# Optimization experiments

Hardware: AMD Instinct MI355X
Metric: run time of the kernel (lower is better)

The kernel has to match this reference:

```python
import jax, jax.numpy as jnp
import numpy as np

TAU = 2.0      # LIF membrane time constant
K = 2          # MaxPool1d kernel/stride
ALPHA = 4.0    # spikingjelly surrogate.Sigmoid default alpha
EPS = 1e-5     # BatchNorm1d eps
VTH = 1.0      # LIF v_threshold default

@jax.custom_vjp
def spike(x):
    # Heaviside forward, sigmoid surrogate gradient (spikingjelly surrogate.Sigmoid)
    return (x >= 0.0).astype(x.dtype)

def _spike_fwd(x):
    return spike(x), x

def _spike_bwd(x, g):
    s = jax.nn.sigmoid(ALPHA * x)
    return (g * ALPHA * s * (1.0 - s),)

spike.defvjp(_spike_fwd, _spike_bwd)


def setup_inputs() -> dict:
    key = jax.random.key(0)
    k1, k2 = jax.random.split(key)
    T, B, N, D, O = 4, 32, 1024, 512, 512
    x = jax.random.normal(k1, (T, B, N, D), jnp.float32)
    W = jax.random.normal(k2, (O, D), jnp.float32) * 0.02
    gamma = jnp.ones((O,), jnp.float32)
    beta = jnp.zeros((O,), jnp.float32)
    running_mean = jnp.zeros((O,), jnp.float32)
    running_var = jnp.ones((O,), jnp.float32)
    return {"x": x, "W": W, "gamma": gamma, "beta": beta,
            "running_mean": running_mean, "running_var": running_var}


def reference(x, W, gamma, beta, running_mean, running_var):
    T, B, N, D = x.shape
    O = W.shape[0]
    # Linear (no bias): [T,B,N,D] x [O,D] -> [T,B,N,O]
    h = jnp.einsum('tbnd,od->tbno', x, W)
    # BatchNorm1d in inference form (running stats), fused affine
    inv = gamma * jax.lax.rsqrt(running_var + EPS)
    h = h * inv + (beta - running_mean * inv)
    # MaxPool1d(kernel_size=K, stride=K) over feature dim -> [T,B,N,O//K]
    h = h.reshape(T, B, N, O // K, K).max(axis=-1)
    # Multi-step LIF: v = v + (x - v)/tau; spike = H(v - vth); hard reset to 0
    def step(v, xt):
        v = v + (xt - v) / TAU
        s = spike(v - VTH)
        v = v * (1.0 - jax.lax.stop_gradient(s))  # detach_reset=True
        return v, s
    _, spikes = jax.lax.scan(step, jnp.zeros_like(h[0]), h)
    return spikes
```

## Files before the change

kernel.cpp:

```cpp
#include <hip/hip_runtime.h>

constexpr int T_ = 4, B_ = 32, N_ = 1024, D_ = 512, O_ = 512, OP_ = 256;
constexpr int M_ = T_ * B_ * N_;
constexpr unsigned CAP = 1u * 1024 * 1024;

constexpr size_t WS_CNT  = 0;
constexpr size_t WS_WP   = 1u << 20;
constexpr size_t WS_LIST = WS_WP + (1u << 20);
constexpr size_t WS_NEED = WS_LIST + (size_t)CAP * 4;

typedef __attribute__((ext_vector_type(8)))  short bf8;
typedef __attribute__((ext_vector_type(16))) float f16v;

union U2B { struct { uint2 a, b; } p; bf8 v; };

__device__ __forceinline__ unsigned cvtpk(float x0, float x1) {
    unsigned r;
    asm("v_cvt_pk_bf16_f32 %0, %1, %2" : "=v"(r) : "v"(x0), "v"(x1));
    return r;
}
__device__ __forceinline__ float hi_lo_f(unsigned u) { return __uint_as_float(u << 16); }
__device__ __forceinline__ float hi_hi_f(unsigned u) { return __uint_as_float(u & 0xffff0000u); }

__global__ __launch_bounds__(256) void k_wprep(const float* __restrict__ W,
                                               unsigned short* __restrict__ wp,
                                               unsigned* __restrict__ cnt)
{
    if (blockIdx.x == 0 && threadIdx.x == 0) *cnt = 0u;
    const int c = blockIdx.x * 256 + threadIdx.x;
    const int lane = c & 63, q = (c >> 6) & 7, j = (c >> 9) & 15, panel = c >> 13;
    const int colblk = panel >> 1, half = panel & 1;
    const int tm = q >> 2, eo = (q >> 1) & 1, Kh = q & 1;
    const int col = colblk * 128 + half * 64 + 2 * (lane & 31) + eo;
    const int k0 = j * 32 + Kh * 16 + (lane >> 5) * 8;
    const float* src = W + (size_t)col * 512 + k0;
    const float4 v0 = *(const float4*)(src);
    const float4 v1 = *(const float4*)(src + 4);
    const float xs[8] = {v0.x, v0.y, v0.z, v0.w, v1.x, v1.y, v1.z, v1.w};
    unsigned o[4];
    #pragma unroll
    for (int p = 0; p < 4; ++p) {
        const unsigned hi = cvtpk(xs[2 * p], xs[2 * p + 1]);
        if (tm == 0) {
            o[p] = hi;
        } else {
            const float l0 = xs[2 * p] - hi_lo_f(hi);
            const float l1 = xs[2 * p + 1] - hi_hi_f(hi);
            o[p] = cvtpk(l0, l1);
        }
    }
    *(uint4*)(wp + (size_t)c * 8) = make_uint4(o[0], o[1], o[2], o[3]);
}

__global__ __launch_bounds__(256, 3) void k_gemm(
    const float* __restrict__ x, const unsigned short* __restrict__ wp,
    const float* __restrict__ gamma, const float* __restrict__ beta,
    const float* __restrict__ rmean, const float* __restrict__ rvar,
    float* __restrict__ out, unsigned* __restrict__ cnt, unsigned* __restrict__ list)
{
    extern __shared__ char lds[];
    const int tid  = threadIdx.x;
    const int lane = tid & 63;
    const int wid  = tid >> 6;

    const int dd = blockIdx.x;
    const int w  = (dd & 7) * 512 + (dd >> 3);
    const int colblk = w & 3, rowblk = w >> 2;
    const int c0  = colblk * 128;
    const int wr0 = (wid >> 1) * 64, wc0 = (wid & 1) * 64;

    const int cE = c0 + wc0 + 2 * (lane & 31);
    const int cO = cE + 1;
    const float invE = gamma[cE] / sqrtf(rvar[cE] + 1e-5f);
    const float addE = beta[cE] - rmean[cE] * invE;
    const float invO = gamma[cO] / sqrtf(rvar[cO] + 1e-5f);
    const float addO = beta[cO] - rmean[cO] * invO;
    asm volatile("s_waitcnt vmcnt(0)" ::: "memory");
    __builtin_amdgcn_sched_barrier(0);

    const int arow = tid >> 1;
    const int kh   = tid & 1;
    const int t_a  = arow & 3;
    const int sl_a = arow >> 2;
    const unsigned vA = (unsigned)(t_a * 32768 + rowblk * 32 + sl_a) * 2048u
                      + (unsigned)kh * 64u;
    const int Xw = (arow >> 1) & 7;
    const int wA0 = arow * 64 + (((4 * kh + 0) ^ Xw) << 3);
    const int wA1 = arow * 64 + (((4 * kh + 1) ^ Xw) << 3);
    const int wA2 = arow * 64 + (((4 * kh + 2) ^ Xw) << 3);
    const int wA3 = arow * 64 + (((4 * kh + 3) ^ Xw) << 3);

    int rA00, rA01, rA10, rA11;
    {
        const int qv = lane & 31, hs = lane >> 5;
        const int Xr = (qv >> 1) & 7;
        const int r0 = wr0 + qv, r1 = wr0 + 32 + qv;
        rA00 = r0 * 64 + (((0 + hs * 2) ^ Xr) << 3);
        rA01 = r0 * 64 + (((4 + hs * 2) ^ Xr) << 3);
        rA10 = r1 * 64 + (((0 + hs * 2) ^ Xr) << 3);
        rA11 = r1 * 64 + (((4 + hs * 2) ^ Xr) << 3);
    }

    const int panel = colblk * 2 + (wid & 1);
    const unsigned vBb = ((unsigned)panel << 17) + (unsigned)lane * 16u;

    f16v accE[2], accO[2];
    #pragma unroll
    for (int i = 0; i < 2; ++i) { accE[i] = (f16v)0.0f; accO[i] = (f16v)0.0f; }

    float4 Aa[4], Ab[4];
    bf8 Bf[8];
    bf8 ah[4];

#define SCHED __builtin_amdgcn_sched_barrier(0)

#define ALOAD(AI, K)                                                              \
    do {                                                                          \
        asm volatile("global_load_dwordx4 %0, %1, %2 offset:%3"                   \
                     : "=v"(AI[0]) : "v"(vA), "s"(x), "n"((K)*128 + 0)  : "memory"); \
        asm volatile("global_load_dwordx4 %0, %1, %2 offset:%3"                   \
                     : "=v"(AI[1]) : "v"(vA), "s"(x), "n"((K)*128 + 16) : "memory"); \
        asm volatile("global_load_dwordx4 %0, %1, %2 offset:%3"                   \
                     : "=v"(AI[2]) : "v"(vA), "s"(x), "n"((K)*128 + 32) : "memory"); \
        asm volatile("global_load_dwordx4 %0, %1, %2 offset:%3"                   \
                     : "=v"(AI[3]) : "v"(vA), "s"(x), "n"((K)*128 + 48) : "memory"); \
    } while (0)

#define BGRP(KH, K)                                                               \
    do {                                                                          \
        const unsigned vk  = vBb + (unsigned)((K) * 8192 + (KH) * 1024);          \
        const unsigned vk2 = vk + 4096u;                                          \
        asm volatile("global_load_dwordx4 %0, %1, %2 offset:%3"                   \
                     : "=v"(Bf[(KH)*4 + 0]) : "v"(vk),  "s"(wp), "n"(0)    : "memory"); \
        asm volatile("global_load_dwordx4 %0, %1, %2 offset:%3"                   \
                     : "=v"(Bf[(KH)*4 + 1]) : "v"(vk),  "s"(wp), "n"(2048) : "memory"); \
        asm volatile("global_load_dwordx4 %0, %1, %2 offset:%3"                   \
                     : "=v"(Bf[(KH)*4 + 2]) : "v"(vk2), "s"(wp), "n"(0)    : "memory"); \
        asm volatile("global_load_dwordx4 %0, %1, %2 offset:%3"                   \
                     : "=v"(Bf[(KH)*4 + 3]) : "v"(vk2), "s"(wp), "n"(2048) : "memory"); \
    } while (0)

#define DSR1(J, IDX, RA)                                                          \
    do {                                                                          \
        const char* bR = lds + ((J) & 1) * 8192;                                  \
        U2B t;                                                                    \
        t.p.a = *(const uint2*)(bR + (RA));                                       \
        t.p.b = *(const uint2*)(bR + ((RA) ^ 8));                                 \
        ah[IDX] = t.v;                                                            \
    } while (0)

#define CONVW(AC, BUF)                                                            \
    do {                                                                          \
        char* pw = lds + (BUF) * 8192;                                            \
        unsigned q0 = cvtpk(AC[0].x, AC[0].y), q1 = cvtpk(AC[0].z, AC[0].w);      \
        unsigned q2 = cvtpk(AC[1].x, AC[1].y), q3 = cvtpk(AC[1].z, AC[1].w);      \
        *(uint2*)(pw + wA0) = make_uint2(q0, q1);                                 \
        *(uint2*)(pw + wA1) = make_uint2(q2, q3);                                 \
        q0 = cvtpk(AC[2].x, AC[2].y); q1 = cvtpk(AC[2].z, AC[2].w);               \
        q2 = cvtpk(AC[3].x, AC[3].y); q3 = cvtpk(AC[3].z, AC[3].w);               \
        *(uint2*)(pw + wA2) = make_uint2(q0, q1);                                 \
        *(uint2*)(pw + wA3) = make_uint2(q2, q3);                                 \
    } while (0)

#define MGRP4(KH, RT)                                                             \
    do {                                                                          \
        accE[RT] = __builtin_amdgcn_mfma_f32_32x32x16_bf16(ah[(RT)*2+(KH)], Bf[(KH)*4+0], accE[RT], 0, 0, 0); \
        accO[RT] = __builtin_amdgcn_mfma_f32_32x32x16_bf16(ah[(RT)*2+(KH)], Bf[(KH)*4+1], accO[RT], 0, 0, 0); \
        accE[RT] = __builtin_amdgcn_mfma_f32_32x32x16_bf16(ah[(RT)*2+(KH)], Bf[(KH)*4+2], accE[RT], 0, 0, 0); \
        accO[RT] = __builtin_amdgcn_mfma_f32_32x32x16_bf16(ah[(RT)*2+(KH)], Bf[(KH)*4+3], accO[RT], 0, 0, 0); \
    } while (0)

#define PRIO1 __builtin_amdgcn_s_setprio(1)
#define PRIO0 __builtin_amdgcn_s_setprio(0)

#define ITER(J, ATGT, ACV)                                                        \
    do {                                                                          \
        SCHED;                                                                    \
        asm volatile("s_waitcnt vmcnt(8)" ::: "memory");        \
        asm volatile("s_waitcnt lgkmcnt(0)" ::: "memory");      \
        __builtin_amdgcn_s_barrier();                                             \
        SCHED;                                                                    \
        DSR1(J, 0, rA00);                                       \
        SCHED;                                                                    \
        asm volatile("s_waitcnt vmcnt(4)" ::: "memory");       \
        SCHED;                                                                    \
        PRIO1; MGRP4(0, 0); PRIO0;                                                \
        SCHED;                                                                    \
        DSR1(J, 2, rA10);                                       \
        if ((J) + 2 <= 15) { ALOAD(ATGT, (J) + 2); }                              \
        SCHED;                                                                    \
        PRIO1; MGRP4(0, 1); PRIO0;                                                \
        SCHED;                                                                    \
        DSR1(J, 1, rA01);                                       \
        DSR1(J, 3, rA11);                                       \
        BGRP(0, (J) + 1);                                                         \
        SCHED;                                                                    \
        asm volatile("s_waitcnt vmcnt(8)" ::: "memory");       \
        SCHED;                                                                    \
        PRIO1; MGRP4(1, 0); PRIO0;                                                \
        SCHED;                                                                    \
        CONVW(ACV, ((J) + 1) & 1);                             \
        SCHED;                                                                    \
        PRIO1; MGRP4(1, 1); PRIO0;                                                \
        SCHED;                                                                    \
        BGRP(1, (J) + 1);                                                         \
        SCHED;                                                                    \
    } while (0)

    SCHED;
    ALOAD(Aa, 0);
    ALOAD(Ab, 1);
    SCHED;
    BGRP(0, 0);
    BGRP(1, 0);
    SCHED;
    asm volatile("s_waitcnt vmcnt(12)" ::: "memory");
    SCHED;
    CONVW(Aa, 0);
    SCHED;

    ITER(0,  Aa, Ab);
    ITER(1,  Ab, Aa);
    ITER(2,  Aa, Ab);
    ITER(3,  Ab, Aa);
    ITER(4,  Aa, Ab);
    ITER(5,  Ab, Aa);
    ITER(6,  Aa, Ab);
    ITER(7,  Ab, Aa);
    ITER(8,  Aa, Ab);
    ITER(9,  Ab, Aa);
    ITER(10, Aa, Ab);
    ITER(11, Ab, Aa);
    ITER(12, Aa, Ab);
    ITER(13, Ab, Aa);

    SCHED;
    asm volatile("s_waitcnt vmcnt(8)" ::: "memory");
    asm volatile("s_waitcnt lgkmcnt(0)" ::: "memory");
    __builtin_amdgcn_s_barrier();
    SCHED;
    DSR1(14, 0, rA00);
    SCHED;
    asm volatile("s_waitcnt vmcnt(4)" ::: "memory");
    SCHED;
    PRIO1; MGRP4(0, 0); PRIO0;
    SCHED;
    DSR1(14, 2, rA10);
    SCHED;
    PRIO1; MGRP4(0, 1); PRIO0;
    SCHED;
    DSR1(14, 1, rA01);
    DSR1(14, 3, rA11);
    BGRP(0, 15);
    SCHED;
    asm volatile("s_waitcnt vmcnt(4)" ::: "memory");
    SCHED;
    PRIO1; MGRP4(1, 0); PRIO0;
    SCHED;
    CONVW(Ab, 1);
    SCHED;
    PRIO1; MGRP4(1, 1); PRIO0;
    SCHED;
    BGRP(1, 15);
    SCHED;

    asm volatile("s_waitcnt lgkmcnt(0)" ::: "memory");
    __builtin_amdgcn_s_barrier();
    SCHED;
    DSR1(15, 0, rA00);
    DSR1(15, 2, rA10);
    SCHED;
    asm volatile("s_waitcnt vmcnt(4)" ::: "memory");
    SCHED;
    PRIO1; MGRP4(0, 0); PRIO0;
    SCHED;
    DSR1(15, 1, rA01);
    DSR1(15, 3, rA11);
    SCHED;
    PRIO1; MGRP4(0, 1); PRIO0;
    SCHED;
    asm volatile("s_waitcnt vmcnt(0)" ::: "memory");
    SCHED;
    PRIO1; MGRP4(1, 0); PRIO0;
    SCHED;
    PRIO1; MGRP4(1, 1); PRIO0;
    SCHED;

#undef ITER
#undef PRIO1
#undef PRIO0
#undef MGRP4
#undef DSR1
#undef CONVW
#undef BGRP
#undef ALOAD
#undef SCHED

    const int opL = ((c0 + wc0) >> 1) + (lane & 31);
    #pragma unroll
    for (int rt = 0; rt < 2; ++rt) {
        #pragma unroll
        for (int g = 0; g < 4; ++g) {
            const int site = rowblk * 32 + (wid >> 1) * 16 + rt * 8 + 2 * g + (lane >> 5);
            const int bI = site >> 10, nI = site & 1023;
            float v = 0.0f;
            bool flg = false;
            #pragma unroll
            for (int t = 0; t < 4; ++t) {
                const float hE = accE[rt][g * 4 + t] * invE + addE;
                const float hO = accO[rt][g * 4 + t] * invO + addO;
                const float m = fmaxf(hE, hO);
                v = (v + m) * 0.5f;
                const float dv = v - 1.0f;
                const bool sp = dv >= 0.0f;
                out[(((size_t)t * 32 + bI) * 1024 + nI) * 256 + opL] = sp ? 1.0f : 0.0f;
                flg |= (fabsf(dv) < 1e-2f);
                if (sp) v = 0.0f;
            }
            if (flg) {
                unsigned idx = atomicAdd(cnt, 1u);
                if (idx < CAP) list[idx] = ((unsigned)site << 8) | (unsigned)opL;
            }
        }
    }
}

__global__ __launch_bounds__(256) void k_repair(
    const float* __restrict__ x, const float* __restrict__ W,
    const float* __restrict__ gamma, const float* __restrict__ beta,
    const float* __restrict__ rmean, const float* __restrict__ rvar,
    float* __restrict__ out, const unsigned* __restrict__ cnt,
    const unsigned* __restrict__ list)
{
    unsigned count = *cnt;
    if (count > CAP) count = CAP;
    const int lane = threadIdx.x & 63;
    const unsigned gw = (blockIdx.x * 256u + threadIdx.x) >> 6;
    const unsigned nw = (gridDim.x * 256u) >> 6;
    const int d0 = lane * 8;

    for (unsigned j = gw; j < count; j += nw) {
        const unsigned e = list[j];
        const int op = e & 255;
        const int site = e >> 8;
        const int bI = site >> 10, nI = site & 1023;

        double wv[2][8];
        #pragma unroll
        for (int p = 0; p < 2; ++p) {
            const float* Wr = W + (size_t)(2 * op + p) * D_ + d0;
            const float4 a = *(const float4*)(Wr);
            const float4 b = *(const float4*)(Wr + 4);
            wv[p][0] = a.x; wv[p][1] = a.y; wv[p][2] = a.z; wv[p][3] = a.w;
            wv[p][4] = b.x; wv[p][5] = b.y; wv[p][6] = b.z; wv[p][7] = b.w;
        }

        double h[4][2];
        #pragma unroll
        for (int t = 0; t < 4; ++t) {
            const float* xr = x + (((size_t)t * 32 + bI) * 1024 + nI) * D_ + d0;
            const float4 a = *(const float4*)(xr);
            const float4 b = *(const float4*)(xr + 4);
            const double xv[8] = {(double)a.x, (double)a.y, (double)a.z, (double)a.w,
                                  (double)b.x, (double)b.y, (double)b.z, (double)b.w};
            #pragma unroll
            for (int p = 0; p < 2; ++p) {
                double s0 = 0, s1 = 0, s2 = 0, s3 = 0;
                s0 = fma(xv[0], wv[p][0], s0); s1 = fma(xv[1], wv[p][1], s1);
                s2 = fma(xv[2], wv[p][2], s2); s3 = fma(xv[3], wv[p][3], s3);
                s0 = fma(xv[4], wv[p][4], s0); s1 = fma(xv[5], wv[p][5], s1);
                s2 = fma(xv[6], wv[p][6], s2); s3 = fma(xv[7], wv[p][7], s3);
                double s = (s0 + s1) + (s2 + s3);
                #pragma unroll
                for (int off = 32; off > 0; off >>= 1)
                    s += __shfl_xor(s, off, 64);
                h[t][p] = s;
            }
        }

        double iv[2], ad[2];
        #pragma unroll
        for (int p = 0; p < 2; ++p) {
            const int c = 2 * op + p;
            iv[p] = (double)gamma[c] / sqrt((double)rvar[c] + 1e-5);
            ad[p] = (double)beta[c] - (double)rmean[c] * iv[p];
        }
        double v = 0.0;
        #pragma unroll
        for (int t = 0; t < 4; ++t) {
            const double h0 = h[t][0] * iv[0] + ad[0];
            const double h1 = h[t][1] * iv[1] + ad[1];
            const double m = fmax(h0, h1);
            v = (v + m) * 0.5;
            const bool sp = (v >= 1.0);
            if (lane == t)
                out[(((size_t)t * 32 + bI) * 1024 + nI) * 256 + op] = sp ? 1.0f : 0.0f;
            if (sp) v = 0.0;
        }
    }
}

constexpr int FB_SITES = 32, FB_ROWS = 128, FB_BN = 64, FB_BK = 16;

__global__ __launch_bounds__(256)
void snn_fused_f64(const float* __restrict__ x, const float* __restrict__ W,
                   const float* __restrict__ gamma, const float* __restrict__ beta,
                   const float* __restrict__ rmean, const float* __restrict__ rvar,
                   float* __restrict__ out)
{
    __shared__ float As[FB_BK][FB_ROWS];
    __shared__ float Bs[FB_BK][FB_BN];
    const int tid = threadIdx.x;
    const int tx = tid & 15, ty = tid >> 4;
    const int c0 = blockIdx.x * FB_BN;
    const int site_base = blockIdx.y * FB_SITES;
    const int b = site_base / N_, n0 = site_base % N_;
    const int lrow = tid >> 1, lk = (tid & 1) * 8;
    const int s_l = lrow >> 2, t_l = lrow & 3;
    const float* xrow = x + (size_t)((t_l * B_ + b) * N_ + (n0 + s_l)) * D_ + lk;
    const int wc = tid & 63, wk = (tid >> 6) * 4;
    const float* wrow = W + (size_t)(c0 + wc) * D_ + wk;
    double acc[8][4];
    #pragma unroll
    for (int i = 0; i < 8; ++i)
        #pragma unroll
        for (int j = 0; j < 4; ++j) acc[i][j] = 0.0;
    for (int k0 = 0; k0 < D_; k0 += FB_BK) {
        const float4 a0 = *(const float4*)(xrow + k0);
        const float4 a1 = *(const float4*)(xrow + k0 + 4);
        const float4 w4 = *(const float4*)(wrow + k0);
        As[lk + 0][lrow] = a0.x; As[lk + 1][lrow] = a0.y; As[lk + 2][lrow] = a0.z; As[lk + 3][lrow] = a0.w;
        As[lk + 4][lrow] = a1.x; As[lk + 5][lrow] = a1.y; As[lk + 6][lrow] = a1.z; As[lk + 7][lrow] = a1.w;
        Bs[wk + 0][wc] = w4.x; Bs[wk + 1][wc] = w4.y; Bs[wk + 2][wc] = w4.z; Bs[wk + 3][wc] = w4.w;
        __syncthreads();
        #pragma unroll
        for (int k = 0; k < FB_BK; ++k) {
            const float4 af0 = *(const float4*)&As[k][ty * 8];
            const float4 af1 = *(const float4*)&As[k][ty * 8 + 4];
            const float4 bf = *(const float4*)&Bs[k][tx * 4];
            const double ad[8] = {(double)af0.x, (double)af0.y, (double)af0.z, (double)af0.w,
                                  (double)af1.x, (double)af1.y, (double)af1.z, (double)af1.w};
            const double bd[4] = {(double)bf.x, (double)bf.y, (double)bf.z, (double)bf.w};
            #pragma unroll
            for (int i = 0; i < 8; ++i)
                #pragma unroll
                for (int j = 0; j < 4; ++j) acc[i][j] = fma(ad[i], bd[j], acc[i][j]);
        }
        __syncthreads();
    }
    double invd[4], addd[4];
    #pragma unroll
    for (int j = 0; j < 4; ++j) {
        const int c = c0 + tx * 4 + j;
        const double ivv = (double)gamma[c] / sqrt((double)rvar[c] + 1e-5);
        invd[j] = ivv; addd[j] = (double)beta[c] - (double)rmean[c] * ivv;
    }
    #pragma unroll
    for (int si = 0; si < 2; ++si) {
        const int n = n0 + ty * 2 + si;
        #pragma unroll
        for (int p = 0; p < 2; ++p) {
            const int op = (c0 >> 1) + tx * 2 + p;
            double v = 0.0;
            #pragma unroll
            for (int t = 0; t < 4; ++t) {
                const int i = si * 4 + t;
                const double h0 = acc[i][2 * p] * invd[2 * p] + addd[2 * p];
                const double h1 = acc[i][2 * p + 1] * invd[2 * p + 1] + addd[2 * p + 1];
                const double m = fmax(h0, h1);
                v = v + (m - v) * 0.5;
                const bool sp = (v >= 1.0);
                out[((size_t)(t * B_ + b) * N_ + n) * OP_ + op] = sp ? 1.0f : 0.0f;
                if (sp) v = 0.0;
            }
        }
    }
}

extern "C" void kernel_launch(void* const* d_in, const int* in_sizes, int n_in,
                              void* d_out, int out_size, void* d_ws, size_t ws_size,
                              hipStream_t stream)
{
    const float* x     = (const float*)d_in[0];
    const float* W     = (const float*)d_in[1];
    const float* gamma = (const float*)d_in[2];
    const float* beta  = (const float*)d_in[3];
    const float* rmean = (const float*)d_in[4];
    const float* rvar  = (const float*)d_in[5];
    float* out = (float*)d_out;

    if (ws_size < WS_NEED) {
        dim3 grid(O_ / FB_BN, (B_ * N_) / FB_SITES);
        snn_fused_f64<<<grid, dim3(256), 0, stream>>>(x, W, gamma, beta, rmean, rvar, out);
        return;
    }

    char* ws = (char*)d_ws;
    unsigned* cnt = (unsigned*)(ws + WS_CNT);
    unsigned short* wp = (unsigned short*)(ws + WS_WP);
    unsigned* list = (unsigned*)(ws + WS_LIST);

    k_wprep<<<256, 256, 0, stream>>>(W, wp, cnt);
    k_gemm<<<4096, 256, 16384, stream>>>(x, wp, gamma, beta, rmean, rvar, out, cnt, list);
    k_repair<<<512, 256, 0, stream>>>(x, W, gamma, beta, rmean, rvar, out, cnt, list);
}
```

Baseline: 204.3 us.

## Split GEMM block tile across eight waves with one 32-row tile each

```diff
diff --git a/kernel.cpp b/kernel.cpp
--- a/kernel.cpp
+++ b/kernel.cpp
@@ -52,7 +52,7 @@
     *(uint4*)(wp + (size_t)c * 8) = make_uint4(o[0], o[1], o[2], o[3]);
 }
 
-__global__ __launch_bounds__(256, 3) void k_gemm(
+__global__ __launch_bounds__(512, 4) void k_gemm(
     const float* __restrict__ x, const unsigned short* __restrict__ wp,
     const float* __restrict__ gamma, const float* __restrict__ beta,
     const float* __restrict__ rmean, const float* __restrict__ rvar,
@@ -67,9 +67,10 @@
     const int w  = (dd & 7) * 512 + (dd >> 3);
     const int colblk = w & 3, rowblk = w >> 2;
     const int c0  = colblk * 128;
-    const int wr0 = (wid >> 1) * 64, wc0 = (wid & 1) * 64;
-
-    const int cE = c0 + wc0 + 2 * (lane & 31);
+    const int wr  = (wid >> 1) * 32;
+    const int wc  = (wid & 1) * 64;
+
+    const int cE = c0 + wc + 2 * (lane & 31);
     const int cO = cE + 1;
     const float invE = gamma[cE] / sqrtf(rvar[cE] + 1e-5f);
     const float addE = beta[cE] - rmean[cE] * invE;
@@ -78,39 +79,32 @@
     asm volatile("s_waitcnt vmcnt(0)" ::: "memory");
     __builtin_amdgcn_sched_barrier(0);
 
-    const int arow = tid >> 1;
-    const int kh   = tid & 1;
-    const int t_a  = arow & 3;
-    const int sl_a = arow >> 2;
+    const int r_s = tid >> 2;
+    const int q_s = tid & 3;
+    const int t_a  = r_s & 3;
+    const int sl_a = r_s >> 2;
     const unsigned vA = (unsigned)(t_a * 32768 + rowblk * 32 + sl_a) * 2048u
-                      + (unsigned)kh * 64u;
-    const int Xw = (arow >> 1) & 7;
-    const int wA0 = arow * 64 + (((4 * kh + 0) ^ Xw) << 3);
-    const int wA1 = arow * 64 + (((4 * kh + 1) ^ Xw) << 3);
-    const int wA2 = arow * 64 + (((4 * kh + 2) ^ Xw) << 3);
-    const int wA3 = arow * 64 + (((4 * kh + 3) ^ Xw) << 3);
-
-    int rA00, rA01, rA10, rA11;
+                      + (unsigned)q_s * 32u;
+    const int Xw = (r_s >> 1) & 7;
+    const int wA0 = r_s * 64 + (((2 * q_s) ^ Xw) << 3);
+
+    int rA0, rA1;
     {
         const int qv = lane & 31, hs = lane >> 5;
         const int Xr = (qv >> 1) & 7;
-        const int r0 = wr0 + qv, r1 = wr0 + 32 + qv;
-        rA00 = r0 * 64 + (((0 + hs * 2) ^ Xr) << 3);
-        rA01 = r0 * 64 + (((4 + hs * 2) ^ Xr) << 3);
-        rA10 = r1 * 64 + (((0 + hs * 2) ^ Xr) << 3);
-        rA11 = r1 * 64 + (((4 + hs * 2) ^ Xr) << 3);
+        const int row = wr + qv;
+        rA0 = row * 64 + (((0 + hs * 2) ^ Xr) << 3);
+        rA1 = row * 64 + (((4 + hs * 2) ^ Xr) << 3);
     }
 
     const int panel = colblk * 2 + (wid & 1);
     const unsigned vBb = ((unsigned)panel << 17) + (unsigned)lane * 16u;
 
-    f16v accE[2], accO[2];
-    #pragma unroll
-    for (int i = 0; i < 2; ++i) { accE[i] = (f16v)0.0f; accO[i] = (f16v)0.0f; }
-
-    float4 Aa[4], Ab[4];
+    f16v accE = (f16v)0.0f, accO = (f16v)0.0f;
+
+    float4 Aa[2], Ab[2];
     bf8 Bf[8];
-    bf8 ah[4];
+    bf8 ah[2];
 
 #define SCHED __builtin_amdgcn_sched_barrier(0)
 
@@ -120,10 +114,6 @@
                      : "=v"(AI[0]) : "v"(vA), "s"(x), "n"((K)*128 + 0)  : "memory"); \
         asm volatile("global_load_dwordx4 %0, %1, %2 offset:%3"                   \
                      : "=v"(AI[1]) : "v"(vA), "s"(x), "n"((K)*128 + 16) : "memory"); \
-        asm volatile("global_load_dwordx4 %0, %1, %2 offset:%3"                   \
-                     : "=v"(AI[2]) : "v"(vA), "s"(x), "n"((K)*128 + 32) : "memory"); \
-        asm volatile("global_load_dwordx4 %0, %1, %2 offset:%3"                   \
-                     : "=v"(AI[3]) : "v"(vA), "s"(x), "n"((K)*128 + 48) : "memory"); \
     } while (0)
 
 #define BGRP(KH, K)                                                               \
@@ -140,34 +130,30 @@
                      : "=v"(Bf[(KH)*4 + 3]) : "v"(vk2), "s"(wp), "n"(2048) : "memory"); \
     } while (0)
 
-#define DSR1(J, IDX, RA)                                                          \
+#define DSR1(J, KH, RA)                                                           \
     do {                                                                          \
         const char* bR = lds + ((J) & 1) * 8192;                                  \
         U2B t;                                                                    \
         t.p.a = *(const uint2*)(bR + (RA));                                       \
         t.p.b = *(const uint2*)(bR + ((RA) ^ 8));                                 \
-        ah[IDX] = t.v;                                                            \
+        ah[KH] = t.v;                                                             \
     } while (0)
 
 #define CONVW(AC, BUF)                                                            \
     do {                                                                          \
         char* pw = lds + (BUF) * 8192;                                            \
-        unsigned q0 = cvtpk(AC[0].x, AC[0].y), q1 = cvtpk(AC[0].z, AC[0].w);      \
-        unsigned q2 = cvtpk(AC[1].x, AC[1].y), q3 = cvtpk(AC[1].z, AC[1].w);      \
+        const unsigned q0 = cvtpk(AC[0].x, AC[0].y), q1 = cvtpk(AC[0].z, AC[0].w);\
+        const unsigned q2 = cvtpk(AC[1].x, AC[1].y), q3 = cvtpk(AC[1].z, AC[1].w);\
         *(uint2*)(pw + wA0) = make_uint2(q0, q1);                                 \
-        *(uint2*)(pw + wA1) = make_uint2(q2, q3);                                 \
-        q0 = cvtpk(AC[2].x, AC[2].y); q1 = cvtpk(AC[2].z, AC[2].w);               \
-        q2 = cvtpk(AC[3].x, AC[3].y); q3 = cvtpk(AC[3].z, AC[3].w);               \
-        *(uint2*)(pw + wA2) = make_uint2(q0, q1);                                 \
-        *(uint2*)(pw + wA3) = make_uint2(q2, q3);                                 \
-    } while (0)
-
-#define MGRP4(KH, RT)                                                             \
-    do {                                                                          \
-        accE[RT] = __builtin_amdgcn_mfma_f32_32x32x16_bf16(ah[(RT)*2+(KH)], Bf[(KH)*4+0], accE[RT], 0, 0, 0); \
-        accO[RT] = __builtin_amdgcn_mfma_f32_32x32x16_bf16(ah[(RT)*2+(KH)], Bf[(KH)*4+1], accO[RT], 0, 0, 0); \
-        accE[RT] = __builtin_amdgcn_mfma_f32_32x32x16_bf16(ah[(RT)*2+(KH)], Bf[(KH)*4+2], accE[RT], 0, 0, 0); \
-        accO[RT] = __builtin_amdgcn_mfma_f32_32x32x16_bf16(ah[(RT)*2+(KH)], Bf[(KH)*4+3], accO[RT], 0, 0, 0); \
+        *(uint2*)(pw + (wA0 ^ 8)) = make_uint2(q2, q3);                           \
+    } while (0)
+
+#define MGRP(KH)                                                                  \
+    do {                                                                          \
+        accE = __builtin_amdgcn_mfma_f32_32x32x16_bf16(ah[KH], Bf[(KH)*4+0], accE, 0, 0, 0); \
+        accO = __builtin_amdgcn_mfma_f32_32x32x16_bf16(ah[KH], Bf[(KH)*4+1], accO, 0, 0, 0); \
+        accE = __builtin_amdgcn_mfma_f32_32x32x16_bf16(ah[KH], Bf[(KH)*4+2], accE, 0, 0, 0); \
+        accO = __builtin_amdgcn_mfma_f32_32x32x16_bf16(ah[KH], Bf[(KH)*4+3], accO, 0, 0, 0); \
     } while (0)
 
 #define PRIO1 __builtin_amdgcn_s_setprio(1)
@@ -180,28 +166,21 @@
         asm volatile("s_waitcnt lgkmcnt(0)" ::: "memory");      \
         __builtin_amdgcn_s_barrier();                                             \
         SCHED;                                                                    \
-        DSR1(J, 0, rA00);                                       \
+        DSR1(J, 0, rA0);                                                          \
         SCHED;                                                                    \
         asm volatile("s_waitcnt vmcnt(4)" ::: "memory");       \
         SCHED;                                                                    \
-        PRIO1; MGRP4(0, 0); PRIO0;                                                \
-        SCHED;                                                                    \
-        DSR1(J, 2, rA10);                                       \
+        PRIO1; MGRP(0); PRIO0;                                                    \
+        SCHED;                                                                    \
+        DSR1(J, 1, rA1);                                                          \
         if ((J) + 2 <= 15) { ALOAD(ATGT, (J) + 2); }                              \
-        SCHED;                                                                    \
-        PRIO1; MGRP4(0, 1); PRIO0;                                                \
-        SCHED;                                                                    \
-        DSR1(J, 1, rA01);                                       \
-        DSR1(J, 3, rA11);                                       \
         BGRP(0, (J) + 1);                                                         \
         SCHED;                                                                    \
-        asm volatile("s_waitcnt vmcnt(8)" ::: "memory");       \
-        SCHED;                                                                    \
-        PRIO1; MGRP4(1, 0); PRIO0;                                                \
+        asm volatile("s_waitcnt vmcnt(6)" ::: "memory");       \
+        SCHED;                                                                    \
+        PRIO1; MGRP(1); PRIO0;                                                    \
         SCHED;                                                                    \
         CONVW(ACV, ((J) + 1) & 1);                             \
-        SCHED;                                                                    \
-        PRIO1; MGRP4(1, 1); PRIO0;                                                \
         SCHED;                                                                    \
         BGRP(1, (J) + 1);                                                         \
         SCHED;                                                                    \
@@ -214,7 +193,7 @@
     BGRP(0, 0);
     BGRP(1, 0);
     SCHED;
-    asm volatile("s_waitcnt vmcnt(12)" ::: "memory");
+    asm volatile("s_waitcnt vmcnt(10)" ::: "memory");
     SCHED;
     CONVW(Aa, 0);
     SCHED;
@@ -239,27 +218,20 @@
     asm volatile("s_waitcnt lgkmcnt(0)" ::: "memory");
     __builtin_amdgcn_s_barrier();
     SCHED;
-    DSR1(14, 0, rA00);
+    DSR1(14, 0, rA0);
     SCHED;
     asm volatile("s_waitcnt vmcnt(4)" ::: "memory");
     SCHED;
-    PRIO1; MGRP4(0, 0); PRIO0;
-    SCHED;
-    DSR1(14, 2, rA10);
-    SCHED;
-    PRIO1; MGRP4(0, 1); PRIO0;
-    SCHED;
-    DSR1(14, 1, rA01);
-    DSR1(14, 3, rA11);
+    PRIO1; MGRP(0); PRIO0;
+    SCHED;
+    DSR1(14, 1, rA1);
     BGRP(0, 15);
     SCHED;
     asm volatile("s_waitcnt vmcnt(4)" ::: "memory");
     SCHED;
-    PRIO1; MGRP4(1, 0); PRIO0;
+    PRIO1; MGRP(1); PRIO0;
     SCHED;
     CONVW(Ab, 1);
-    SCHED;
-    PRIO1; MGRP4(1, 1); PRIO0;
     SCHED;
     BGRP(1, 15);
     SCHED;
@@ -267,60 +239,51 @@
     asm volatile("s_waitcnt lgkmcnt(0)" ::: "memory");
     __builtin_amdgcn_s_barrier();
     SCHED;
-    DSR1(15, 0, rA00);
-    DSR1(15, 2, rA10);
+    DSR1(15, 0, rA0);
     SCHED;
     asm volatile("s_waitcnt vmcnt(4)" ::: "memory");
     SCHED;
-    PRIO1; MGRP4(0, 0); PRIO0;
-    SCHED;
-    DSR1(15, 1, rA01);
-    DSR1(15, 3, rA11);
-    SCHED;
-    PRIO1; MGRP4(0, 1); PRIO0;
+    PRIO1; MGRP(0); PRIO0;
+    SCHED;
+    DSR1(15, 1, rA1);
     SCHED;
     asm volatile("s_waitcnt vmcnt(0)" ::: "memory");
     SCHED;
-    PRIO1; MGRP4(1, 0); PRIO0;
-    SCHED;
-    PRIO1; MGRP4(1, 1); PRIO0;
+    PRIO1; MGRP(1); PRIO0;
     SCHED;
 
 #undef ITER
 #undef PRIO1
 #undef PRIO0
-#undef MGRP4
+#undef MGRP
 #undef DSR1
 #undef CONVW
 #undef BGRP
 #undef ALOAD
 #undef SCHED
 
-    const int opL = ((c0 + wc0) >> 1) + (lane & 31);
+    const int opL = ((c0 + wc) >> 1) + (lane & 31);
     #pragma unroll
-    for (int rt = 0; rt < 2; ++rt) {
-        #pragma unroll
-        for (int g = 0; g < 4; ++g) {
-            const int site = rowblk * 32 + (wid >> 1) * 16 + rt * 8 + 2 * g + (lane >> 5);
-            const int bI = site >> 10, nI = site & 1023;
-            float v = 0.0f;
-            bool flg = false;
-            #pragma unroll
-            for (int t = 0; t < 4; ++t) {
-                const float hE = accE[rt][g * 4 + t] * invE + addE;
-                const float hO = accO[rt][g * 4 + t] * invO + addO;
-                const float m = fmaxf(hE, hO);
-                v = (v + m) * 0.5f;
-                const float dv = v - 1.0f;
-                const bool sp = dv >= 0.0f;
-                out[(((size_t)t * 32 + bI) * 1024 + nI) * 256 + opL] = sp ? 1.0f : 0.0f;
-                flg |= (fabsf(dv) < 1e-2f);
-                if (sp) v = 0.0f;
-            }
-            if (flg) {
-                unsigned idx = atomicAdd(cnt, 1u);
-                if (idx < CAP) list[idx] = ((unsigned)site << 8) | (unsigned)opL;
-            }
+    for (int g = 0; g < 4; ++g) {
+        const int site = rowblk * 32 + (wid >> 1) * 8 + 2 * g + (lane >> 5);
+        const int bI = site >> 10, nI = site & 1023;
+        float v = 0.0f;
+        bool flg = false;
+        #pragma unroll
+        for (int t = 0; t < 4; ++t) {
+            const float hE = accE[g * 4 + t] * invE + addE;
+            const float hO = accO[g * 4 + t] * invO + addO;
+            const float m = fmaxf(hE, hO);
+            v = (v + m) * 0.5f;
+            const float dv = v - 1.0f;
+            const bool sp = dv >= 0.0f;
+            out[(((size_t)t * 32 + bI) * 1024 + nI) * 256 + opL] = sp ? 1.0f : 0.0f;
+            flg |= (fabsf(dv) < 1e-2f);
+            if (sp) v = 0.0f;
+        }
+        if (flg) {
+            unsigned idx = atomicAdd(cnt, 1u);
+            if (idx < CAP) list[idx] = ((unsigned)site << 8) | (unsigned)opL;
         }
     }
 }
@@ -501,6 +464,6 @@
     unsigned* list = (unsigned*)(ws + WS_LIST);
 
     k_wprep<<<256, 256, 0, stream>>>(W, wp, cnt);
-    k_gemm<<<4096, 256, 16384, stream>>>(x, wp, gamma, beta, rmean, rvar, out, cnt, list);
+    k_gemm<<<4096, 512, 16384, stream>>>(x, wp, gamma, beta, rmean, rvar, out, cnt, list);
     k_repair<<<512, 256, 0, stream>>>(x, W, gamma, beta, rmean, rvar, out, cnt, list);
 }
```

Measured after the change: 247.6 us. 1.21x slower.
